# Performance work log

Measured on AMD Instinct MI355X. Metric: run time of the kernel, lower is better.

## Reference

```python
import jax, jax.numpy as jnp
import numpy as np

N = 100_000          # NEURON_COUNT (scaled)
INPUT_SIZE = 1024    # input neurons occupy indices [0, INPUT_SIZE)
OUTPUT_SIZE = 256    # output neurons occupy indices [N-OUTPUT_SIZE, N)
E = 10_000_000       # SYNAPSE_RATIO * N
STEPS = 3


def setup_inputs() -> dict:
    key = jax.random.key(0)
    k1, k2, k3, k4, k5 = jax.random.split(key, 5)
    x = jax.random.normal(k1, (INPUT_SIZE,), dtype=jnp.float32)
    synapse_weights = jax.random.normal(k2, (E,), dtype=jnp.float32)
    neuron_biases = jax.random.normal(k3, (N - INPUT_SIZE,), dtype=jnp.float32)
    synapse_src = jax.random.randint(k4, (E,), 0, N, dtype=jnp.int64) if jax.config.jax_enable_x64 else jax.random.randint(k4, (E,), 0, N, dtype=jnp.int32)
    synapse_dst = jax.random.randint(k5, (E,), 0, N, dtype=jnp.int64) if jax.config.jax_enable_x64 else jax.random.randint(k5, (E,), 0, N, dtype=jnp.int32)
    return {
        "x": x,
        "synapse_weights": synapse_weights,
        "neuron_biases": neuron_biases,
        "synapse_src": synapse_src,
        "synapse_dst": synapse_dst,
    }


def reference(x, synapse_weights, neuron_biases, synapse_src, synapse_dst):
    # Initial state: zeros everywhere, inputs injected at the first INPUT_SIZE slots.
    v = jnp.zeros((N,), dtype=x.dtype).at[:INPUT_SIZE].set(x.reshape(-1))
    # tanh applied to all neurons except outputs (last OUTPUT_SIZE indices)
    tanh_mask = jnp.arange(N) < (N - OUTPUT_SIZE)
    for _ in range(STEPS):
        # vectorized gather-multiply-scatter: next[to] += v[from] * w  (one segment_sum)
        msg = v[synapse_src] * synapse_weights                       # [E]
        nxt = jax.ops.segment_sum(msg, synapse_dst, num_segments=N)  # [N]
        # biases added to all non-input neurons
        nxt = nxt.at[INPUT_SIZE:].add(neuron_biases)
        # tanh everywhere except output neurons
        v = jnp.where(tanh_mask, jnp.tanh(nxt), nxt)
    return v[N - OUTPUT_SIZE:]
```

## Files before the change

kernel.cpp:

```cpp
#include <hip/hip_runtime.h>

#define N_NEURONS   100000
#define INPUT_SIZE  1024
#define OUTPUT_SIZE 256
#define E_SYN       10000000
#define STEPS       3

#define RANGES      8
#define BIN         12500
#define SCAT_BLK    1024
#define CBLK        64
#define RG          8
#define RSL         (CBLK / RG)
#define CAP         1280000
#define RB_BLK      256
#define RB_WAVES    4
#define CH          8192
#define B_CNT       1221
#define STG_CAP     128
#define VEC4        (E_SYN / 4)

__global__ void init_all(const float* __restrict__ x, float* __restrict__ v,
                         int* __restrict__ gcur) {
    int i = blockIdx.x * blockDim.x + threadIdx.x;
    if (i < N_NEURONS) v[i] = (i < INPUT_SIZE) ? x[i] : 0.0f;
    if (i < RANGES) gcur[i] = 0;
}

__global__ __launch_bounds__(RB_BLK) void reorder_partition(
        const float* __restrict__ w,
        const int*   __restrict__ src,
        const int*   __restrict__ dst,
        int2* __restrict__ recs,
        int*  __restrict__ gcur) {
    __shared__ int cnt[RANGES];
    __shared__ int blk_cur[RANGES];
    __shared__ int2 stg[RB_WAVES][RANGES][STG_CAP];
    const int tid  = threadIdx.x;
    const int lane = tid & 63;
    const int wv   = tid >> 6;
    const unsigned long long ltmask = (1ull << lane) - 1ull;
    if (tid < RANGES) cnt[tid] = 0;
    __syncthreads();

    const long beg = (long)blockIdx.x * CH;
    const int4* dst4 = (const int4*)dst;
    const int4* src4 = (const int4*)src;
    const int4* wq4  = (const int4*)w;
    const int ITER = CH / (RB_BLK * 4);

    {
        int h[RANGES] = {0, 0, 0, 0, 0, 0, 0, 0};
        for (int it = 0; it < ITER; ++it) {
            long e  = beg + (long)it * RB_BLK * 4 + (long)tid * 4;
            bool ok = (e < E_SYN);
            int4 d4 = ok ? dst4[e >> 2] : make_int4(0, 0, 0, 0);
            unsigned long long okm = __ballot(ok);
            int rk[4] = {d4.x / BIN, d4.y / BIN, d4.z / BIN, d4.w / BIN};
#pragma unroll
            for (int k = 0; k < 4; ++k) {
                unsigned long long b0 = __ballot(rk[k] & 1);
                unsigned long long b1 = __ballot(rk[k] & 2);
                unsigned long long b2 = __ballot(rk[k] & 4);
#pragma unroll
                for (int rr = 0; rr < RANGES; ++rr) {
                    unsigned long long m = ((rr & 1) ? b0 : ~b0) &
                                           ((rr & 2) ? b1 : ~b1) &
                                           ((rr & 4) ? b2 : ~b2) & okm;
                    h[rr] += __popcll(m);
                }
            }
        }
        if (lane < RANGES) {
            int t = h[0];
#pragma unroll
            for (int rr = 1; rr < RANGES; ++rr) if (lane == rr) t = h[rr];
            atomicAdd(&cnt[lane], t);
        }
    }
    __syncthreads();
    if (tid < RANGES) blk_cur[tid] = tid * CAP + atomicAdd(&gcur[tid], cnt[tid]);
    __syncthreads();

    int wr[RANGES] = {0, 0, 0, 0, 0, 0, 0, 0};
    int fl[RANGES] = {0, 0, 0, 0, 0, 0, 0, 0};
    for (int it = 0; it < ITER; ++it) {
        long e  = beg + (long)it * RB_BLK * 4 + (long)tid * 4;
        bool ok = (e < E_SYN);
        int4 d4 = ok ? dst4[e >> 2] : make_int4(0, 0, 0, 0);
        int4 s4 = ok ? src4[e >> 2] : make_int4(0, 0, 0, 0);
        int4 q4 = ok ? wq4[e >> 2]  : make_int4(0, 0, 0, 0);
        unsigned long long okm = __ballot(ok);
        int dd[4] = {d4.x, d4.y, d4.z, d4.w};
        int ss[4] = {s4.x, s4.y, s4.z, s4.w};
        int qq[4] = {q4.x, q4.y, q4.z, q4.w};
#pragma unroll
        for (int k = 0; k < 4; ++k) {
            int r = dd[k] / BIN;
            unsigned long long b0 = __ballot(r & 1);
            unsigned long long b1 = __ballot(r & 2);
            unsigned long long b2 = __ballot(r & 4);
            unsigned long long mym = ((r & 1) ? b0 : ~b0) &
                                     ((r & 2) ? b1 : ~b1) &
                                     ((r & 4) ? b2 : ~b2) & okm;
            int rank = __popcll(mym & ltmask);
            int base = wr[0];
            base = (r == 1) ? wr[1] : base;
            base = (r == 2) ? wr[2] : base;
            base = (r == 3) ? wr[3] : base;
            base = (r == 4) ? wr[4] : base;
            base = (r == 5) ? wr[5] : base;
            base = (r == 6) ? wr[6] : base;
            base = (r == 7) ? wr[7] : base;
            int slot = (base + rank) & (STG_CAP - 1);
            if (ok) stg[wv][r][slot] = make_int2((ss[k] << 14) | (dd[k] - r * BIN), qq[k]);
#pragma unroll
            for (int rr = 0; rr < RANGES; ++rr) {
                unsigned long long m = ((rr & 1) ? b0 : ~b0) &
                                       ((rr & 2) ? b1 : ~b1) &
                                       ((rr & 4) ? b2 : ~b2) & okm;
                wr[rr] += __popcll(m);
            }
#pragma unroll
            for (int rr = 0; rr < RANGES; ++rr) {
                if (wr[rr] - fl[rr] >= 64) {
                    int gpos = 0;
                    if (lane == 0) gpos = atomicAdd(&blk_cur[rr], 64);
                    gpos = __shfl(gpos, 0, 64);
                    int2 rec = stg[wv][rr][(fl[rr] & (STG_CAP - 1)) + lane];
                    recs[(size_t)gpos + lane] = rec;
                    fl[rr] += 64;
                }
            }
        }
    }
#pragma unroll
    for (int rr = 0; rr < RANGES; ++rr) {
        int pend = wr[rr] - fl[rr];
        if (pend > 0) {
            int gpos = 0;
            if (lane == 0) gpos = atomicAdd(&blk_cur[rr], pend);
            gpos = __shfl(gpos, 0, 64);
            if (lane < pend) {
                int2 rec = stg[wv][rr][(fl[rr] & (STG_CAP - 1)) + lane];
                recs[(size_t)gpos + lane] = rec;
            }
        }
    }
}

__global__ __launch_bounds__(SCAT_BLK) void scatter_sorted(
        const int2* __restrict__ recs,
        const int*  __restrict__ gcur,
        const float* __restrict__ v,
        float* __restrict__ partials) {
    __shared__ float bins[BIN];
    const int r = blockIdx.x / CBLK;
    const int c = blockIdx.x % CBLK;
    for (int j = threadIdx.x; j < BIN; j += SCAT_BLK) bins[j] = 0.0f;
    __syncthreads();

    const int cnt   = gcur[r];
    const int npair = cnt >> 1;
    const int4* base4 = (const int4*)(recs + (size_t)r * CAP);
    const int stride = CBLK * SCAT_BLK;
    int u = c * SCAT_BLK + threadIdx.x;
    for (; u + 3 * stride < npair; u += 4 * stride) {
        int4 a = base4[u];
        int4 b = base4[u + stride];
        int4 e = base4[u + 2 * stride];
        int4 f = base4[u + 3 * stride];
        float va0 = v[a.x >> 14];
        float va1 = v[a.z >> 14];
        float vb0 = v[b.x >> 14];
        float vb1 = v[b.z >> 14];
        float ve0 = v[e.x >> 14];
        float ve1 = v[e.z >> 14];
        float vf0 = v[f.x >> 14];
        float vf1 = v[f.z >> 14];
        atomicAdd(&bins[a.x & 16383], va0 * __int_as_float(a.y));
        atomicAdd(&bins[a.z & 16383], va1 * __int_as_float(a.w));
        atomicAdd(&bins[b.x & 16383], vb0 * __int_as_float(b.y));
        atomicAdd(&bins[b.z & 16383], vb1 * __int_as_float(b.w));
        atomicAdd(&bins[e.x & 16383], ve0 * __int_as_float(e.y));
        atomicAdd(&bins[e.z & 16383], ve1 * __int_as_float(e.w));
        atomicAdd(&bins[f.x & 16383], vf0 * __int_as_float(f.y));
        atomicAdd(&bins[f.z & 16383], vf1 * __int_as_float(f.w));
    }
    for (; u < npair; u += stride) {
        int4 a = base4[u];
        atomicAdd(&bins[a.x & 16383], v[a.x >> 14] * __int_as_float(a.y));
        atomicAdd(&bins[a.z & 16383], v[a.z >> 14] * __int_as_float(a.w));
    }
    if ((cnt & 1) && c == 0 && threadIdx.x == 0) {
        int2 p = recs[(size_t)r * CAP + cnt - 1];
        atomicAdd(&bins[p.x & 16383], v[p.x >> 14] * __int_as_float(p.y));
    }
    __syncthreads();
    float* o = partials + (size_t)(r * CBLK + c) * BIN;
    for (int j = threadIdx.x; j < BIN; j += SCAT_BLK) o[j] = bins[j];
}

__global__ void reduce_stage1(const float* __restrict__ partials,
                              float* __restrict__ p2) {
    int i4 = 4 * (blockIdx.x * blockDim.x + threadIdx.x);
    if (i4 >= N_NEURONS) return;
    const int g = blockIdx.y;
    const int r = i4 / BIN;
    const int j = i4 - r * BIN;
    const float* base = partials + ((size_t)(r * CBLK + g * RSL)) * BIN + j;
    float4 acc = {0.f, 0.f, 0.f, 0.f};
#pragma unroll
    for (int c = 0; c < RSL; ++c) {
        float4 p = *(const float4*)(base + (size_t)c * BIN);
        acc.x += p.x; acc.y += p.y; acc.z += p.z; acc.w += p.w;
    }
    *(float4*)(p2 + (size_t)g * N_NEURONS + i4) = acc;
}

__global__ void reduce_stage2(const float* __restrict__ p2,
                              const float* __restrict__ bias,
                              float* __restrict__ v,
                              float* __restrict__ out,
                              int write_out) {
    int i4 = 4 * (blockIdx.x * blockDim.x + threadIdx.x);
    if (i4 >= N_NEURONS) return;
    float4 acc = {0.f, 0.f, 0.f, 0.f};
#pragma unroll
    for (int g = 0; g < RG; ++g) {
        float4 p = *(const float4*)(p2 + (size_t)g * N_NEURONS + i4);
        acc.x += p.x; acc.y += p.y; acc.z += p.z; acc.w += p.w;
    }
    float av[4] = {acc.x, acc.y, acc.z, acc.w};
#pragma unroll
    for (int k = 0; k < 4; ++k) {
        int i = i4 + k;
        float val = av[k] + ((i >= INPUT_SIZE) ? bias[i - INPUT_SIZE] : 0.0f);
        float nv  = (i < N_NEURONS - OUTPUT_SIZE) ? tanhf(val) : val;
        v[i] = nv;
        if (write_out && i >= N_NEURONS - OUTPUT_SIZE)
            out[i - (N_NEURONS - OUTPUT_SIZE)] = val;
    }
}

__global__ void init_state_fb(const float* __restrict__ x, float* __restrict__ v) {
    int i = blockIdx.x * blockDim.x + threadIdx.x;
    if (i < N_NEURONS) v[i] = (i < INPUT_SIZE) ? x[i] : 0.0f;
}
__global__ void scatter_binned(const float* __restrict__ w,
                               const int*   __restrict__ src,
                               const int*   __restrict__ dst,
                               const float* __restrict__ v,
                               float*       __restrict__ partials,
                               int C) {
    __shared__ float bins[BIN];
    const int r = blockIdx.x / C;
    const int c = blockIdx.x % C;
    const int lo = r * BIN;
    const int hi = lo + BIN;
    for (int j = threadIdx.x; j < BIN; j += blockDim.x) bins[j] = 0.0f;
    __syncthreads();
    const int4*   src4 = (const int4*)src;
    const int4*   dst4 = (const int4*)dst;
    const float4* w4v  = (const float4*)w;
    const int stride = C * blockDim.x;
    for (int u = c * blockDim.x + threadIdx.x; u < VEC4; u += stride) {
        const int4   s4 = src4[u];
        const int4   d4 = dst4[u];
        const float4 wv = w4v[u];
        int   s[4] = {s4.x, s4.y, s4.z, s4.w};
        int   d[4] = {d4.x, d4.y, d4.z, d4.w};
        float ww[4] = {wv.x, wv.y, wv.z, wv.w};
#pragma unroll
        for (int k = 0; k < 4; ++k)
            if (d[k] >= lo && d[k] < hi)
                atomicAdd(&bins[d[k] - lo], v[s[k]] * ww[k]);
    }
    __syncthreads();
    float* o = partials + ((size_t)(r * C + c)) * BIN;
    for (int j = threadIdx.x; j < BIN; j += blockDim.x) o[j] = bins[j];
}
__global__ void reduce_update_fb(const float* __restrict__ partials,
                                 const float* __restrict__ bias,
                                 float* __restrict__ v,
                                 float* __restrict__ out,
                                 int C, int write_out) {
    int i4 = 4 * (blockIdx.x * blockDim.x + threadIdx.x);
    if (i4 >= N_NEURONS) return;
    const int r = i4 / BIN;
    const int j = i4 - r * BIN;
    const float* base = partials + ((size_t)r * C) * BIN + j;
    float4 acc = {0.f, 0.f, 0.f, 0.f};
    for (int c = 0; c < C; ++c) {
        float4 p = *(const float4*)(base + (size_t)c * BIN);
        acc.x += p.x; acc.y += p.y; acc.z += p.z; acc.w += p.w;
    }
    float av[4] = {acc.x, acc.y, acc.z, acc.w};
#pragma unroll
    for (int k = 0; k < 4; ++k) {
        int i = i4 + k;
        float val = av[k] + ((i >= INPUT_SIZE) ? bias[i - INPUT_SIZE] : 0.0f);
        float nv  = (i < N_NEURONS - OUTPUT_SIZE) ? tanhf(val) : val;
        v[i] = nv;
        if (write_out && i >= N_NEURONS - OUTPUT_SIZE)
            out[i - (N_NEURONS - OUTPUT_SIZE)] = val;
    }
}

extern "C" void kernel_launch(void* const* d_in, const int* in_sizes, int n_in,
                              void* d_out, int out_size, void* d_ws, size_t ws_size,
                              hipStream_t stream) {
    const float* x    = (const float*)d_in[0];
    const float* w    = (const float*)d_in[1];
    const float* bias = (const float*)d_in[2];
    const int*   src  = (const int*)d_in[3];
    const int*   dst  = (const int*)d_in[4];
    float* out = (float*)d_out;

    const int blk = 256;
    const int grid_n   = (N_NEURONS + blk - 1) / blk;
    const int red_grid = (N_NEURONS / 4 + blk - 1) / blk;

    float* v        = (float*)d_ws;
    float* partials = v + N_NEURONS;
    float* p2       = partials + (size_t)RANGES * CBLK * BIN;
    int2*  recs     = (int2*)(p2 + (size_t)RG * N_NEURONS);
    int*   gcur     = (int*)(recs + (size_t)RANGES * CAP);
    size_t need = (size_t)((char*)(gcur + RANGES) - (char*)d_ws);

    if (ws_size >= need) {
        init_all<<<grid_n, blk, 0, stream>>>(x, v, gcur);
        reorder_partition<<<B_CNT, RB_BLK, 0, stream>>>(w, src, dst, recs, gcur);
        for (int s = 0; s < STEPS; ++s) {
            scatter_sorted<<<RANGES * CBLK, SCAT_BLK, 0, stream>>>(
                recs, gcur, v, partials);
            reduce_stage1<<<dim3(red_grid, RG), blk, 0, stream>>>(partials, p2);
            reduce_stage2<<<red_grid, blk, 0, stream>>>(
                p2, bias, v, out, s == STEPS - 1 ? 1 : 0);
        }
    } else {
        long C = (long)(ws_size / 4 / N_NEURONS) - 1;
        if (C > 64) C = 64;
        if (C < 1) C = 1;
        float* part_fb = v + N_NEURONS;
        init_state_fb<<<grid_n, blk, 0, stream>>>(x, v);
        for (int s = 0; s < STEPS; ++s) {
            scatter_binned<<<RANGES * (int)C, SCAT_BLK, 0, stream>>>(
                w, src, dst, v, part_fb, (int)C);
            reduce_update_fb<<<red_grid, blk, 0, stream>>>(
                part_fb, bias, v, out, (int)C, s == STEPS - 1 ? 1 : 0);
        }
    }
}
```

Before: 399.4 us.

## Replace atomic-based partition with histogram+scan+per-wave partition; fuse two-stage reduce

The single reorder_partition kernel, which counted per block and reserved output space with global atomics, is split into three kernels. A per-wave-chunk histogram kernel, a scan kernel that computes deterministic per-chunk base offsets, and a partition kernel write records with per-lane range cursors and ballot-driven flushes. The two-stage reduction of partials is fused into one kernel, which removes the intermediate p2 buffer and one launch per step. The new path adds two launches and reads dst twice, but removes global atomics and lets many smaller waves run in parallel.

```diff
diff --git a/kernel.cpp b/kernel.cpp
--- a/kernel.cpp
+++ b/kernel.cpp
@@ -13,79 +13,118 @@
 #define RG          8
 #define RSL         (CBLK / RG)
 #define CAP         1280000
-#define RB_BLK      256
-#define RB_WAVES    4
-#define CH          8192
-#define B_CNT       1221
 #define STG_CAP     128
 #define VEC4        (E_SYN / 4)
 
-__global__ void init_all(const float* __restrict__ x, float* __restrict__ v,
-                         int* __restrict__ gcur) {
+#define CHK         2048
+#define NCH         4883
+#define PITER       (CHK / (64 * 4))
+#define HIST_GRID   ((NCH + 3) / 4)
+#define PART_GRID   ((NCH + 1) / 2)
+
+__global__ void init_state(const float* __restrict__ x, float* __restrict__ v) {
     int i = blockIdx.x * blockDim.x + threadIdx.x;
     if (i < N_NEURONS) v[i] = (i < INPUT_SIZE) ? x[i] : 0.0f;
-    if (i < RANGES) gcur[i] = 0;
-}
-
-__global__ __launch_bounds__(RB_BLK) void reorder_partition(
+}
+
+__global__ __launch_bounds__(256) void hist_kernel(const int* __restrict__ dst,
+                                                   int* __restrict__ hist) {
+    const int lane  = threadIdx.x & 63;
+    const int wv    = threadIdx.x >> 6;
+    const int chunk = blockIdx.x * 4 + wv;
+    if (chunk >= NCH) return;
+    const long beg = (long)chunk * CHK;
+    const int4* dst4 = (const int4*)dst;
+    int h = 0;
+    for (int it = 0; it < PITER; ++it) {
+        long e  = beg + (long)(it * 64 + lane) * 4;
+        bool ok = (e < E_SYN);
+        int4 d4 = ok ? dst4[e >> 2] : make_int4(0, 0, 0, 0);
+        unsigned long long okm = __ballot(ok);
+        int rk[4] = {d4.x / BIN, d4.y / BIN, d4.z / BIN, d4.w / BIN};
+#pragma unroll
+        for (int k = 0; k < 4; ++k) {
+            unsigned long long b0 = __ballot(rk[k] & 1);
+            unsigned long long b1 = __ballot(rk[k] & 2);
+            unsigned long long b2 = __ballot(rk[k] & 4);
+            unsigned long long m = ((lane & 1) ? b0 : ~b0) &
+                                   ((lane & 2) ? b1 : ~b1) &
+                                   ((lane & 4) ? b2 : ~b2) & okm;
+            h += __popcll(m);
+        }
+    }
+    if (lane < RANGES) hist[(size_t)lane * NCH + chunk] = h;
+}
+
+__global__ __launch_bounds__(1024) void scan_kernel(const int* __restrict__ hist,
+                                                    int* __restrict__ bases,
+                                                    int* __restrict__ gcur) {
+    const int r = blockIdx.x;
+    const int t = threadIdx.x;
+    const int lane = t & 63;
+    const int wv   = t >> 6;
+    int vals[5];
+    int s = 0;
+#pragma unroll
+    for (int j = 0; j < 5; ++j) {
+        int idx = t * 5 + j;
+        int vv  = (idx < NCH) ? hist[(size_t)r * NCH + idx] : 0;
+        vals[j] = vv;
+        s += vv;
+    }
+    int x = s;
+#pragma unroll
+    for (int d = 1; d < 64; d <<= 1) {
+        int y = __shfl_up(x, d, 64);
+        if (lane >= d) x += y;
+    }
+    __shared__ int wsum[16];
+    if (lane == 63) wsum[wv] = x;
+    __syncthreads();
+    if (wv == 0) {
+        int y = (lane < 16) ? wsum[lane] : 0;
+        int z = y;
+#pragma unroll
+        for (int d = 1; d < 16; d <<= 1) {
+            int u = __shfl_up(z, d, 64);
+            if (lane >= d) z += u;
+        }
+        if (lane < 16) wsum[lane] = z - y;
+    }
+    __syncthreads();
+    int run = (x - s) + wsum[wv];
+#pragma unroll
+    for (int j = 0; j < 5; ++j) {
+        int idx = t * 5 + j;
+        if (idx < NCH) bases[(size_t)r * NCH + idx] = r * CAP + run;
+        run += vals[j];
+    }
+    if (t == 1023) gcur[r] = run;
+}
+
+__global__ __launch_bounds__(128) void partition_kernel(
         const float* __restrict__ w,
         const int*   __restrict__ src,
         const int*   __restrict__ dst,
-        int2* __restrict__ recs,
-        int*  __restrict__ gcur) {
-    __shared__ int cnt[RANGES];
-    __shared__ int blk_cur[RANGES];
-    __shared__ int2 stg[RB_WAVES][RANGES][STG_CAP];
-    const int tid  = threadIdx.x;
-    const int lane = tid & 63;
-    const int wv   = tid >> 6;
+        const int*   __restrict__ bases,
+        int2* __restrict__ recs) {
+    __shared__ int2 stg[2][RANGES][STG_CAP];
+    const int lane  = threadIdx.x & 63;
+    const int wv    = threadIdx.x >> 6;
+    const int chunk = blockIdx.x * 2 + wv;
+    if (chunk >= NCH) return;
     const unsigned long long ltmask = (1ull << lane) - 1ull;
-    if (tid < RANGES) cnt[tid] = 0;
-    __syncthreads();
-
-    const long beg = (long)blockIdx.x * CH;
+
+    int cur = 0, wrr = 0, flr = 0;
+    if (lane < RANGES) cur = bases[(size_t)lane * NCH + chunk];
+
+    const long beg = (long)chunk * CHK;
     const int4* dst4 = (const int4*)dst;
     const int4* src4 = (const int4*)src;
     const int4* wq4  = (const int4*)w;
-    const int ITER = CH / (RB_BLK * 4);
-
-    {
-        int h[RANGES] = {0, 0, 0, 0, 0, 0, 0, 0};
-        for (int it = 0; it < ITER; ++it) {
-            long e  = beg + (long)it * RB_BLK * 4 + (long)tid * 4;
-            bool ok = (e < E_SYN);
-            int4 d4 = ok ? dst4[e >> 2] : make_int4(0, 0, 0, 0);
-            unsigned long long okm = __ballot(ok);
-            int rk[4] = {d4.x / BIN, d4.y / BIN, d4.z / BIN, d4.w / BIN};
-#pragma unroll
-            for (int k = 0; k < 4; ++k) {
-                unsigned long long b0 = __ballot(rk[k] & 1);
-                unsigned long long b1 = __ballot(rk[k] & 2);
-                unsigned long long b2 = __ballot(rk[k] & 4);
-#pragma unroll
-                for (int rr = 0; rr < RANGES; ++rr) {
-                    unsigned long long m = ((rr & 1) ? b0 : ~b0) &
-                                           ((rr & 2) ? b1 : ~b1) &
-                                           ((rr & 4) ? b2 : ~b2) & okm;
-                    h[rr] += __popcll(m);
-                }
-            }
-        }
-        if (lane < RANGES) {
-            int t = h[0];
-#pragma unroll
-            for (int rr = 1; rr < RANGES; ++rr) if (lane == rr) t = h[rr];
-            atomicAdd(&cnt[lane], t);
-        }
-    }
-    __syncthreads();
-    if (tid < RANGES) blk_cur[tid] = tid * CAP + atomicAdd(&gcur[tid], cnt[tid]);
-    __syncthreads();
-
-    int wr[RANGES] = {0, 0, 0, 0, 0, 0, 0, 0};
-    int fl[RANGES] = {0, 0, 0, 0, 0, 0, 0, 0};
-    for (int it = 0; it < ITER; ++it) {
-        long e  = beg + (long)it * RB_BLK * 4 + (long)tid * 4;
+
+    for (int it = 0; it < PITER; ++it) {
+        long e  = beg + (long)(it * 64 + lane) * 4;
         bool ok = (e < E_SYN);
         int4 d4 = ok ? dst4[e >> 2] : make_int4(0, 0, 0, 0);
         int4 s4 = ok ? src4[e >> 2] : make_int4(0, 0, 0, 0);
@@ -96,55 +135,43 @@
         int qq[4] = {q4.x, q4.y, q4.z, q4.w};
 #pragma unroll
         for (int k = 0; k < 4; ++k) {
-            int r = dd[k] / BIN;
+            int d = dd[k];
+            int r = d / BIN;
             unsigned long long b0 = __ballot(r & 1);
             unsigned long long b1 = __ballot(r & 2);
             unsigned long long b2 = __ballot(r & 4);
             unsigned long long mym = ((r & 1) ? b0 : ~b0) &
                                      ((r & 2) ? b1 : ~b1) &
                                      ((r & 4) ? b2 : ~b2) & okm;
-            int rank = __popcll(mym & ltmask);
-            int base = wr[0];
-            base = (r == 1) ? wr[1] : base;
-            base = (r == 2) ? wr[2] : base;
-            base = (r == 3) ? wr[3] : base;
-            base = (r == 4) ? wr[4] : base;
-            base = (r == 5) ? wr[5] : base;
-            base = (r == 6) ? wr[6] : base;
-            base = (r == 7) ? wr[7] : base;
-            int slot = (base + rank) & (STG_CAP - 1);
-            if (ok) stg[wv][r][slot] = make_int2((ss[k] << 14) | (dd[k] - r * BIN), qq[k]);
-#pragma unroll
-            for (int rr = 0; rr < RANGES; ++rr) {
-                unsigned long long m = ((rr & 1) ? b0 : ~b0) &
-                                       ((rr & 2) ? b1 : ~b1) &
-                                       ((rr & 4) ? b2 : ~b2) & okm;
-                wr[rr] += __popcll(m);
+            int rank  = __popcll(mym & ltmask);
+            int wslot = __shfl(wrr, r, 64);
+            int slot  = (wslot + rank) & (STG_CAP - 1);
+            if (ok) stg[wv][r][slot] = make_int2((ss[k] << 14) | (d - r * BIN), qq[k]);
+            unsigned long long mm = ((lane & 1) ? b0 : ~b0) &
+                                    ((lane & 2) ? b1 : ~b1) &
+                                    ((lane & 4) ? b2 : ~b2) & okm;
+            wrr += __popcll(mm);
+            unsigned long long fb = __ballot(wrr - flr >= 64) & 0xFFull;
+            while (fb) {
+                int rr = __ffsll((long long)fb) - 1;
+                fb &= fb - 1;
+                int gpos = __shfl(cur, rr, 64);
+                int f0   = __shfl(flr, rr, 64) & (STG_CAP - 1);
+                int2 rec = stg[wv][rr][f0 + lane];
+                recs[(size_t)gpos + lane] = rec;
+                if (lane == rr) { flr += 64; cur += 64; }
             }
-#pragma unroll
-            for (int rr = 0; rr < RANGES; ++rr) {
-                if (wr[rr] - fl[rr] >= 64) {
-                    int gpos = 0;
-                    if (lane == 0) gpos = atomicAdd(&blk_cur[rr], 64);
-                    gpos = __shfl(gpos, 0, 64);
-                    int2 rec = stg[wv][rr][(fl[rr] & (STG_CAP - 1)) + lane];
-                    recs[(size_t)gpos + lane] = rec;
-                    fl[rr] += 64;
-                }
-            }
         }
     }
 #pragma unroll
     for (int rr = 0; rr < RANGES; ++rr) {
-        int pend = wr[rr] - fl[rr];
+        int wt = __shfl(wrr, rr, 64);
+        int ft = __shfl(flr, rr, 64);
+        int pend = wt - ft;
         if (pend > 0) {
-            int gpos = 0;
-            if (lane == 0) gpos = atomicAdd(&blk_cur[rr], pend);
-            gpos = __shfl(gpos, 0, 64);
-            if (lane < pend) {
-                int2 rec = stg[wv][rr][(fl[rr] & (STG_CAP - 1)) + lane];
-                recs[(size_t)gpos + lane] = rec;
-            }
+            int gpos = __shfl(cur, rr, 64);
+            if (lane < pend)
+                recs[(size_t)gpos + lane] = stg[wv][rr][(ft & (STG_CAP - 1)) + lane];
         }
     }
 }
@@ -201,37 +228,28 @@
     for (int j = threadIdx.x; j < BIN; j += SCAT_BLK) o[j] = bins[j];
 }
 
-__global__ void reduce_stage1(const float* __restrict__ partials,
-                              float* __restrict__ p2) {
+__global__ void reduce_fused(const float* __restrict__ partials,
+                             const float* __restrict__ bias,
+                             float* __restrict__ v,
+                             float* __restrict__ out,
+                             int write_out) {
     int i4 = 4 * (blockIdx.x * blockDim.x + threadIdx.x);
     if (i4 >= N_NEURONS) return;
-    const int g = blockIdx.y;
     const int r = i4 / BIN;
     const int j = i4 - r * BIN;
-    const float* base = partials + ((size_t)(r * CBLK + g * RSL)) * BIN + j;
-    float4 acc = {0.f, 0.f, 0.f, 0.f};
-#pragma unroll
-    for (int c = 0; c < RSL; ++c) {
-        float4 p = *(const float4*)(base + (size_t)c * BIN);
-        acc.x += p.x; acc.y += p.y; acc.z += p.z; acc.w += p.w;
-    }
-    *(float4*)(p2 + (size_t)g * N_NEURONS + i4) = acc;
-}
-
-__global__ void reduce_stage2(const float* __restrict__ p2,
-                              const float* __restrict__ bias,
-                              float* __restrict__ v,
-                              float* __restrict__ out,
-                              int write_out) {
-    int i4 = 4 * (blockIdx.x * blockDim.x + threadIdx.x);
-    if (i4 >= N_NEURONS) return;
-    float4 acc = {0.f, 0.f, 0.f, 0.f};
-#pragma unroll
+    const float* base = partials + (size_t)(r * CBLK) * BIN + j;
+    float4 tot = {0.f, 0.f, 0.f, 0.f};
+#pragma unroll 2
     for (int g = 0; g < RG; ++g) {
-        float4 p = *(const float4*)(p2 + (size_t)g * N_NEURONS + i4);
-        acc.x += p.x; acc.y += p.y; acc.z += p.z; acc.w += p.w;
-    }
-    float av[4] = {acc.x, acc.y, acc.z, acc.w};
+        float4 a = {0.f, 0.f, 0.f, 0.f};
+#pragma unroll
+        for (int cc = 0; cc < RSL; ++cc) {
+            float4 p = *(const float4*)(base + (size_t)(g * RSL + cc) * BIN);
+            a.x += p.x; a.y += p.y; a.z += p.z; a.w += p.w;
+        }
+        tot.x += a.x; tot.y += a.y; tot.z += a.z; tot.w += a.w;
+    }
+    float av[4] = {tot.x, tot.y, tot.z, tot.w};
 #pragma unroll
     for (int k = 0; k < 4; ++k) {
         int i = i4 + k;
@@ -243,10 +261,6 @@
     }
 }
 
-__global__ void init_state_fb(const float* __restrict__ x, float* __restrict__ v) {
-    int i = blockIdx.x * blockDim.x + threadIdx.x;
-    if (i < N_NEURONS) v[i] = (i < INPUT_SIZE) ? x[i] : 0.0f;
-}
 __global__ void scatter_binned(const float* __restrict__ w,
                                const int*   __restrict__ src,
                                const int*   __restrict__ dst,
@@ -323,27 +337,29 @@
 
     float* v        = (float*)d_ws;
     float* partials = v + N_NEURONS;
-    float* p2       = partials + (size_t)RANGES * CBLK * BIN;
-    int2*  recs     = (int2*)(p2 + (size_t)RG * N_NEURONS);
+    int*   hist     = (int*)(partials + (size_t)RANGES * CBLK * BIN);
+    int*   bases    = hist + (size_t)RANGES * NCH;
+    int2*  recs     = (int2*)(bases + (size_t)RANGES * NCH);
     int*   gcur     = (int*)(recs + (size_t)RANGES * CAP);
     size_t need = (size_t)((char*)(gcur + RANGES) - (char*)d_ws);
 
     if (ws_size >= need) {
-        init_all<<<grid_n, blk, 0, stream>>>(x, v, gcur);
-        reorder_partition<<<B_CNT, RB_BLK, 0, stream>>>(w, src, dst, recs, gcur);
+        init_state<<<grid_n, blk, 0, stream>>>(x, v);
+        hist_kernel<<<HIST_GRID, 256, 0, stream>>>(dst, hist);
+        scan_kernel<<<RANGES, 1024, 0, stream>>>(hist, bases, gcur);
+        partition_kernel<<<PART_GRID, 128, 0, stream>>>(w, src, dst, bases, recs);
         for (int s = 0; s < STEPS; ++s) {
             scatter_sorted<<<RANGES * CBLK, SCAT_BLK, 0, stream>>>(
                 recs, gcur, v, partials);
-            reduce_stage1<<<dim3(red_grid, RG), blk, 0, stream>>>(partials, p2);
-            reduce_stage2<<<red_grid, blk, 0, stream>>>(
-                p2, bias, v, out, s == STEPS - 1 ? 1 : 0);
+            reduce_fused<<<red_grid, blk, 0, stream>>>(
+                partials, bias, v, out, s == STEPS - 1 ? 1 : 0);
         }
     } else {
         long C = (long)(ws_size / 4 / N_NEURONS) - 1;
         if (C > 64) C = 64;
         if (C < 1) C = 1;
         float* part_fb = v + N_NEURONS;
-        init_state_fb<<<grid_n, blk, 0, stream>>>(x, v);
+        init_state<<<grid_n, blk, 0, stream>>>(x, v);
         for (int s = 0; s < STEPS; ++s) {
             scatter_binned<<<RANGES * (int)C, SCAT_BLK, 0, stream>>>(
                 w, src, dst, v, part_fb, (int)C);
```

Result: faster. 378.1 us (-5.3%).
